# Kernel optimization log

Hardware: AMD Instinct MI355X
Metric: run time of the kernel (lower is better)

The kernel has to match this reference:

```python
import jax, jax.numpy as jnp
import numpy as np

V, E, SH, H = 10004, 300, 1024, 512
B, T = 128, 50
PAD = 10003


def setup_inputs() -> dict:
    key = jax.random.key(0)
    ks = jax.random.split(key, 13)
    s = 0.05
    emb = s * jax.random.normal(ks[0], (V, E), dtype=jnp.float32)
    emb = emb.at[PAD].set(0.0)  # padding_idx row is zero
    G = 2 * H  # GRU hidden size is 2*hid_size
    Wih = s * jax.random.normal(ks[1], (3 * G, E), dtype=jnp.float32)
    Whh = s * jax.random.normal(ks[2], (3 * G, G), dtype=jnp.float32)
    bih = s * jax.random.normal(ks[3], (3 * G,), dtype=jnp.float32)
    bhh = s * jax.random.normal(ks[4], (3 * G,), dtype=jnp.float32)
    W1 = s * jax.random.normal(ks[5], (H, SH), dtype=jnp.float32)
    b1 = s * jax.random.normal(ks[6], (H,), dtype=jnp.float32)
    W2 = s * jax.random.normal(ks[7], (E, G), dtype=jnp.float32)
    b2 = s * jax.random.normal(ks[8], (E,), dtype=jnp.float32)
    Wout = s * jax.random.normal(ks[9], (V, E), dtype=jnp.float32)
    ses_encoding = jax.random.normal(ks[10], (1, B, SH), dtype=jnp.float32)
    x = jax.random.randint(ks[11], (B, T), 0, 10000)
    return {"ses_encoding": ses_encoding, "x": x, "emb": emb, "Wih": Wih,
            "Whh": Whh, "bih": bih, "bhh": bhh, "W1": W1, "b1": b1,
            "W2": W2, "b2": b2, "Wout": Wout}


def reference(ses_encoding, x, emb, Wih, Whh, bih, bhh, W1, b1, W2, b2, Wout):
    hid = W1.shape[0]            # hid_size
    G = Whh.shape[1]             # 2*hid_size (GRU hidden)
    # ses_encoding = tanh(lin1(ses_encoding)), then viewed to [1, B, hid]
    ses = jnp.tanh(jnp.einsum('lbs,hs->lbh', ses_encoding, W1) + b1)[0]  # [B, hid]
    emb_all = emb[x]             # [B, T, E] (dropout inactive at eval)

    def step(h, e_t):
        # GRU hidden input each step: concat(prev_half, ses) -> [B, 2*hid]
        Hfull = jnp.concatenate([h, ses], axis=-1)
        gx = e_t @ Wih.T + bih                      # [B, 3G]
        gh = Hfull @ Whh.T + bhh                    # [B, 3G]
        r = jax.nn.sigmoid(gx[:, :G] + gh[:, :G])
        z = jax.nn.sigmoid(gx[:, G:2 * G] + gh[:, G:2 * G])
        n = jnp.tanh(gx[:, 2 * G:] + r * gh[:, 2 * G:])
        hnew = (1.0 - z) * n + z * Hfull            # [B, 2*hid]
        o = hnew @ W2.T + b2 + e_t                  # lin2(hid_o) + residual emb
        logits = o @ Wout.T                         # [B, V]
        return hnew[:, :hid], logits

    _, logits = jax.lax.scan(step, ses, jnp.swapaxes(emb_all, 0, 1))
    return jnp.swapaxes(logits, 0, 1)               # [B, T, V]
```

## Files before the change

### kernel.cpp

```cpp
#include <hip/hip_runtime.h>


typedef __bf16 bf16x8 __attribute__((ext_vector_type(8)));
typedef float f32x4 __attribute__((ext_vector_type(4)));
typedef unsigned long long u64;

struct CvtAll {
    const float* src[7];
    int srows[7], scols[7], sstride[7], soff[7], drows[7], dcols[7];
    __bf16* dst[7];
    int blk0[8];
    const int* x; const float* emb; __bf16* embbf;
};

__global__ void cvt_all_kernel(CvtAll p) {
    int bid = blockIdx.x;
    if (bid >= p.blk0[7]) {
        int idx = (bid - p.blk0[7]) * 256 + threadIdx.x;
        if (idx >= 6400 * 320) return;
        int m = idx / 320, c = idx - m * 320;
        int t = m >> 7, b = m & 127;
        int tok = p.x[b * 50 + t];
        float v = (c < 300) ? p.emb[(size_t)tok * 300 + c] : 0.0f;
        p.embbf[idx] = (__bf16)v;
        return;
    }
    int s = 0;
    while (s < 6 && bid >= p.blk0[s + 1]) ++s;
    int idx = (bid - p.blk0[s]) * 256 + threadIdx.x;
    int dc = p.dcols[s];
    int r = idx / dc, c = idx - r * dc;
    if (r >= p.drows[s]) return;
    float v = 0.0f;
    if (r < p.srows[s] && c < p.scols[s])
        v = p.src[s][(size_t)r * p.sstride[s] + p.soff[s] + c];
    p.dst[s][(size_t)r * dc + c] = (__bf16)v;
}

struct GemmParams {
    const __bf16* A; int lda;
    const __bf16* B; int ldb; int Brows;
    int K;
    const float* bias;
    float* outF; int ldo; int Nstore;
    __bf16* outBf;
    const __bf16* res;
    const float* add2;
    int ld2; int add2lim;
};

template <int EPI>
__launch_bounds__(256, 2)
__global__ void gemm_bt(GemmParams p) {
    __shared__ __bf16 As[128][72];
    __shared__ __bf16 Bs[128][72];

    const int tid = threadIdx.x;
    const int lane = tid & 63;
    const int wid = tid >> 6;
    const int wr = wid >> 1, wc = wid & 1;
    const int m0 = blockIdx.x * 128, c0 = blockIdx.y * 128;
    const int lrow = lane & 15;
    const int kq = lane >> 4;

    int srow[4], scol[4];
#pragma unroll
    for (int i = 0; i < 4; ++i) {
        int chunk = i * 256 + tid;
        srow[i] = chunk >> 3;
        scol[i] = (chunk & 7) * 8;
    }

    f32x4 acc[4][4];
#pragma unroll
    for (int i = 0; i < 4; ++i)
#pragma unroll
        for (int j = 0; j < 4; ++j) acc[i][j] = (f32x4){0.f, 0.f, 0.f, 0.f};

    const int nkb = p.K >> 6;
    bf16x8 ra[4], rb[4];
#pragma unroll
    for (int i = 0; i < 4; ++i) {
        ra[i] = *reinterpret_cast<const bf16x8*>(
            p.A + (size_t)(m0 + srow[i]) * p.lda + scol[i]);
        bf16x8 z;
#pragma unroll
        for (int q = 0; q < 8; ++q) z[q] = (__bf16)0.0f;
        int grow = c0 + srow[i];
        rb[i] = (grow < p.Brows)
            ? *reinterpret_cast<const bf16x8*>(p.B + (size_t)grow * p.ldb + scol[i])
            : z;
    }

    for (int kb = 0; kb < nkb; ++kb) {
        __syncthreads();
#pragma unroll
        for (int i = 0; i < 4; ++i) {
            *reinterpret_cast<bf16x8*>(&As[srow[i]][scol[i]]) = ra[i];
            *reinterpret_cast<bf16x8*>(&Bs[srow[i]][scol[i]]) = rb[i];
        }
        __syncthreads();

        if (kb + 1 < nkb) {
            int ko = (kb + 1) << 6;
#pragma unroll
            for (int i = 0; i < 4; ++i) {
                ra[i] = *reinterpret_cast<const bf16x8*>(
                    p.A + (size_t)(m0 + srow[i]) * p.lda + ko + scol[i]);
                bf16x8 z;
#pragma unroll
                for (int q = 0; q < 8; ++q) z[q] = (__bf16)0.0f;
                int grow = c0 + srow[i];
                rb[i] = (grow < p.Brows)
                    ? *reinterpret_cast<const bf16x8*>(
                          p.B + (size_t)grow * p.ldb + ko + scol[i])
                    : z;
            }
        }

#pragma unroll
        for (int kk = 0; kk < 2; ++kk) {
            bf16x8 af[4], bfr[4];
#pragma unroll
            for (int m = 0; m < 4; ++m)
                af[m] = *reinterpret_cast<const bf16x8*>(
                    &As[wr * 64 + m * 16 + lrow][kk * 32 + kq * 8]);
#pragma unroll
            for (int n = 0; n < 4; ++n)
                bfr[n] = *reinterpret_cast<const bf16x8*>(
                    &Bs[wc * 64 + n * 16 + lrow][kk * 32 + kq * 8]);
#pragma unroll
            for (int m = 0; m < 4; ++m)
#pragma unroll
                for (int n = 0; n < 4; ++n)
                    acc[m][n] = __builtin_amdgcn_mfma_f32_16x16x32_bf16(
                        af[m], bfr[n], acc[m][n], 0, 0, 0);
        }
    }

#pragma unroll
    for (int m = 0; m < 4; ++m) {
#pragma unroll
        for (int n = 0; n < 4; ++n) {
#pragma unroll
            for (int i = 0; i < 4; ++i) {
                int r = m0 + wr * 64 + m * 16 + kq * 4 + i;
                int c = c0 + wc * 64 + n * 16 + lrow;
                float v = acc[m][n][i];
                if constexpr (EPI == 1) {
                    v = tanhf(v + p.bias[c]);
                    p.outBf[(size_t)r * p.ldo + c] = (__bf16)v;
                    p.outF[(size_t)c * 128 + r] = v;
                } else if constexpr (EPI == 2) {
                    int ro = (r & 127) * 50 + (r >> 7);
                    if (c < 300) {
                        v += p.bias[c] + (float)p.res[(size_t)r * 320 + c];
                        p.outBf[(size_t)ro * 320 + c] = (__bf16)v;
                    } else if (c < 320) {
                        p.outBf[(size_t)ro * 320 + c] = (__bf16)0.0f;
                    }
                } else if constexpr (EPI == 3) {
                    if (c < p.Nstore) p.outF[(size_t)r * p.ldo + c] = v;
                } else {
                    if (c < p.Brows) {
                        float v2 = v + p.bias[r];
                        if (p.add2 && r < p.add2lim)
                            v2 += p.add2[(size_t)r * 128 + (c & 127)];
                        p.outF[(size_t)(c >> 7) * p.ldo + (size_t)r * 128 + (c & 127)] = v2;
                    }
                }
            }
        }
    }
}

#define SCAN_NB 64
__launch_bounds__(256, 1)
__global__ void scan_kernel(const __bf16* __restrict__ Whh_a,
                            const float* __restrict__ gxT,
                            const float* __restrict__ ghcT,
                            const float* __restrict__ sesT,
                            u64* __restrict__ F,
                            unsigned* __restrict__ cnt) {
    __shared__ char smem[131072];
    char* Ws = smem;
    char* Hs = smem + 98304;
    const int tid = threadIdx.x;
    const int lane = tid & 63;
    const int wid = tid >> 6;
    const int wr = wid >> 1, wc = wid & 1;
    const int bid = blockIdx.x;
    const int q = bid >> 4;
    const int j0 = (bid & 15) * 32;
    const int lrow = lane & 15, kq = lane >> 4;

    for (int it = 0; it < 24; ++it) {
        int c = it * 256 + tid;
        int rl = c >> 6, o16 = c & 63;
        int g = rl >> 5, jj = rl & 31;
        bf16x8 v = *reinterpret_cast<const bf16x8*>(
            Whh_a + (size_t)(g * 1024 + j0 + jj) * 512 + o16 * 8);
        *reinterpret_cast<bf16x8*>(Ws + rl * 1024 + ((o16 * 16) ^ ((rl & 7) << 4))) = v;
    }

    const int b_g = q * 32 + wc * 16 + lrow;
    const int jbase = j0 + wr * 16 + kq * 4;

    float cn[4], hprev[4], gcur[12], gpre[12];
#pragma unroll
    for (int i = 0; i < 4; ++i) {
        cn[i] = ghcT[(size_t)(2048 + jbase + i) * 128 + b_g];
        hprev[i] = sesT[(size_t)(jbase + i) * 128 + b_g];
    }
#pragma unroll
    for (int i = 0; i < 4; ++i) {
        gpre[i]     = gxT[(size_t)(jbase + i) * 128 + b_g];
        gpre[4 + i] = gxT[(size_t)(1024 + jbase + i) * 128 + b_g];
        gpre[8 + i] = gxT[(size_t)(2048 + jbase + i) * 128 + b_g];
    }

    for (int t = 0; t < 50; ++t) {
        for (int it = 0; it < 16; ++it) {
            int c = it * 256 + tid;
            int rl = c >> 7, o8 = c & 127;
            u64 v = __hip_atomic_load(
                F + ((size_t)t * 128 + q * 32 + rl) * 256 + o8,
                __ATOMIC_RELAXED, __HIP_MEMORY_SCOPE_AGENT);
            *reinterpret_cast<u64*>(Hs + rl * 1024 + ((o8 * 8) ^ ((rl & 7) << 4))) = v;
        }
#pragma unroll
        for (int i = 0; i < 12; ++i) gcur[i] = gpre[i];
        {
            int tn = (t < 49) ? t + 1 : 49;
            const float* gxt = gxT + (size_t)tn * 3072 * 128;
#pragma unroll
            for (int i = 0; i < 4; ++i) {
                gpre[i]     = gxt[(size_t)(jbase + i) * 128 + b_g];
                gpre[4 + i] = gxt[(size_t)(1024 + jbase + i) * 128 + b_g];
                gpre[8 + i] = gxt[(size_t)(2048 + jbase + i) * 128 + b_g];
            }
        }
        asm volatile("s_waitcnt lgkmcnt(0)\n\ts_barrier" ::: "memory");
        __builtin_amdgcn_sched_barrier(0);

        f32x4 acc[3];
#pragma unroll
        for (int g = 0; g < 3; ++g) acc[g] = (f32x4){0.f, 0.f, 0.f, 0.f};
        const int hrow = wc * 16 + lrow;
        const int arow0 = wr * 16 + lrow;
        for (int kb = 0; kb < 16; ++kb) {
            int ko = kb * 64 + kq * 16;
            bf16x8 hfrag = *reinterpret_cast<const bf16x8*>(
                Hs + hrow * 1024 + (ko ^ ((hrow & 7) << 4)));
#pragma unroll
            for (int g = 0; g < 3; ++g) {
                int arow = g * 32 + arow0;
                bf16x8 wfrag = *reinterpret_cast<const bf16x8*>(
                    Ws + arow * 1024 + (ko ^ ((arow & 7) << 4)));
                acc[g] = __builtin_amdgcn_mfma_f32_16x16x32_bf16(
                    wfrag, hfrag, acc[g], 0, 0, 0);
            }
        }

        union { u64 u; __bf16 h[4]; } pk;
#pragma unroll
        for (int i = 0; i < 4; ++i) {
            float r = 1.0f / (1.0f + expf(-(gcur[i] + acc[0][i])));
            float z = 1.0f / (1.0f + expf(-(gcur[4 + i] + acc[1][i])));
            float nn = tanhf(gcur[8 + i] + r * (acc[2][i] + cn[i]));
            float hn = (1.0f - z) * nn + z * hprev[i];
            hprev[i] = hn;
            pk.h[i] = (__bf16)hn;
        }
        __hip_atomic_store(
            F + ((size_t)(t + 1) * 128 + b_g) * 256 + (jbase >> 2), pk.u,
            __ATOMIC_RELAXED, __HIP_MEMORY_SCOPE_AGENT);

        if (t < 49) {
            __syncthreads();
            if (tid == 0) {
                __hip_atomic_fetch_add(cnt + q * 32, 1u,
                                       __ATOMIC_RELAXED, __HIP_MEMORY_SCOPE_AGENT);
                unsigned tgt = (unsigned)(t + 1) * 16u;
                while (__hip_atomic_load(cnt + q * 32, __ATOMIC_RELAXED,
                                         __HIP_MEMORY_SCOPE_AGENT) < tgt)
                    __builtin_amdgcn_s_sleep(1);
            }
            __syncthreads();
        }
    }
}

__launch_bounds__(256, 1)
__global__ void tail_kernel(const __bf16* __restrict__ Whh_a,
                            const float* __restrict__ gxT,
                            const float* __restrict__ ghcT,
                            const float* __restrict__ sesT,
                            __bf16* __restrict__ F) {
    __shared__ char smem[131072];
    char* Ws = smem;
    char* Hs = smem + 98304;
    const int tid = threadIdx.x;
    const int lane = tid & 63;
    const int wid = tid >> 6;
    const int wr = wid >> 1, wc = wid & 1;
    const int bid = blockIdx.x;
    const int tseg = bid >> 6;
    const int rem = bid & 63;
    const int q = rem >> 4;
    const int j0 = 512 + (rem & 15) * 32;
    const int lrow = lane & 15, kq = lane >> 4;

    const int t0 = (tseg < 2) ? tseg * 13 : 26 + (tseg - 2) * 12;
    const int t1 = (tseg < 2) ? t0 + 13 : t0 + 12;

    for (int it = 0; it < 24; ++it) {
        int c = it * 256 + tid;
        int rl = c >> 6, o16 = c & 63;
        int g = rl >> 5, jj = rl & 31;
        bf16x8 v = *reinterpret_cast<const bf16x8*>(
            Whh_a + (size_t)(g * 1024 + j0 + jj) * 512 + o16 * 8);
        *reinterpret_cast<bf16x8*>(Ws + rl * 1024 + ((o16 * 16) ^ ((rl & 7) << 4))) = v;
    }

    const int b_g = q * 32 + wc * 16 + lrow;
    const int jbase = j0 + wr * 16 + kq * 4;

    float cn[4], sv[4];
#pragma unroll
    for (int i = 0; i < 4; ++i) {
        cn[i] = ghcT[(size_t)(2048 + jbase + i) * 128 + b_g];
        sv[i] = sesT[(size_t)(jbase + i - 512) * 128 + b_g];
    }

    for (int tt = t0; tt < t1; ++tt) {
        for (int it = 0; it < 8; ++it) {
            int c = it * 256 + tid;
            int rl = c >> 6, o16 = c & 63;
            bf16x8 v = *reinterpret_cast<const bf16x8*>(
                F + ((size_t)tt * 128 + q * 32 + rl) * 1024 + o16 * 8);
            *reinterpret_cast<bf16x8*>(Hs + rl * 1024 + ((o16 * 16) ^ ((rl & 7) << 4))) = v;
        }
        const float* gxt = gxT + (size_t)tt * 3072 * 128;
        float g0[12];
#pragma unroll
        for (int i = 0; i < 4; ++i) {
            g0[i]     = gxt[(size_t)(jbase + i) * 128 + b_g];
            g0[4 + i] = gxt[(size_t)(1024 + jbase + i) * 128 + b_g];
            g0[8 + i] = gxt[(size_t)(2048 + jbase + i) * 128 + b_g];
        }
        __syncthreads();

        f32x4 acc[3];
#pragma unroll
        for (int g = 0; g < 3; ++g) acc[g] = (f32x4){0.f, 0.f, 0.f, 0.f};
        const int hrow = wc * 16 + lrow;
        const int arow0 = wr * 16 + lrow;
        for (int kb = 0; kb < 16; ++kb) {
            int ko = kb * 64 + kq * 16;
            bf16x8 hfrag = *reinterpret_cast<const bf16x8*>(
                Hs + hrow * 1024 + (ko ^ ((hrow & 7) << 4)));
#pragma unroll
            for (int g = 0; g < 3; ++g) {
                int arow = g * 32 + arow0;
                bf16x8 wfrag = *reinterpret_cast<const bf16x8*>(
                    Ws + arow * 1024 + (ko ^ ((arow & 7) << 4)));
                acc[g] = __builtin_amdgcn_mfma_f32_16x16x32_bf16(
                    wfrag, hfrag, acc[g], 0, 0, 0);
            }
        }

        union { u64 u; __bf16 h[4]; } pk;
#pragma unroll
        for (int i = 0; i < 4; ++i) {
            float r = 1.0f / (1.0f + expf(-(g0[i] + acc[0][i])));
            float z = 1.0f / (1.0f + expf(-(g0[4 + i] + acc[1][i])));
            float nn = tanhf(g0[8 + i] + r * (acc[2][i] + cn[i]));
            pk.h[i] = (__bf16)((1.0f - z) * nn + z * sv[i]);
        }
        *reinterpret_cast<u64*>(F + ((size_t)(tt + 1) * 128 + b_g) * 1024 + jbase) = pk.u;
        __syncthreads();
    }
}

extern "C" void kernel_launch(void* const* d_in, const int* in_sizes, int n_in,
                              void* d_out, int out_size, void* d_ws, size_t ws_size,
                              hipStream_t stream) {
    const float* ses_enc = (const float*)d_in[0];
    const int*   x       = (const int*)d_in[1];
    const float* emb     = (const float*)d_in[2];
    const float* Wih     = (const float*)d_in[3];
    const float* Whh     = (const float*)d_in[4];
    const float* bih     = (const float*)d_in[5];
    const float* bhh     = (const float*)d_in[6];
    const float* W1      = (const float*)d_in[7];
    const float* b1      = (const float*)d_in[8];
    const float* W2      = (const float*)d_in[9];
    const float* b2      = (const float*)d_in[10];
    const float* Wout    = (const float*)d_in[11];
    float* out = (float*)d_out;

    char* ws = (char*)d_ws;
    float*  sesT      = (float*)(ws + 0);
    float*  ghcT      = (float*)(ws + 262144);
    __bf16* o_bf      = (__bf16*)(ws + 1835008);
    __bf16* W1_bf     = (__bf16*)(ws + 5931008);
    __bf16* Whh_a_bf  = (__bf16*)(ws + 6979584);
    __bf16* Whh_b_bf  = (__bf16*)(ws + 10125312);
    __bf16* Wih_bf    = (__bf16*)(ws + 13271040);
    __bf16* W2_bf     = (__bf16*)(ws + 15237120);
    __bf16* Wout_bf   = (__bf16*)(ws + 15851520);
    __bf16* sesenc_bf = (__bf16*)(ws + 22323200);
    unsigned* cnt     = (unsigned*)(ws + 22585344);

    char* ob = (char*)d_out;
    float*  gxT     = (float*)ob;
    __bf16* emb_bf  = (__bf16*)(ob + 80000000);
    __bf16* F       = (__bf16*)(ob + 88000000);

    dim3 blk(256);

    CvtAll ca;
    const float* csrc[7]  = {W1, Whh, Whh, Wih, W2, Wout, ses_enc};
    int csr[7]  = {512, 3072, 3072, 3072, 300, 10004, 128};
    int csc[7]  = {1024, 512, 512, 300, 1024, 300, 1024};
    int cst[7]  = {1024, 1024, 1024, 300, 1024, 300, 1024};
    int cso[7]  = {0, 0, 512, 0, 0, 0, 0};
    __bf16* cdst[7] = {W1_bf, Whh_a_bf, Whh_b_bf, Wih_bf, W2_bf, Wout_bf, sesenc_bf};
    int cdr[7]  = {512, 3072, 3072, 3072, 300, 10112, 128};
    int cdc[7]  = {1024, 512, 512, 320, 1024, 320, 1024};
    int b0 = 0;
    for (int s = 0; s < 7; ++s) {
        ca.src[s] = csrc[s]; ca.srows[s] = csr[s]; ca.scols[s] = csc[s];
        ca.sstride[s] = cst[s]; ca.soff[s] = cso[s];
        ca.dst[s] = cdst[s]; ca.drows[s] = cdr[s]; ca.dcols[s] = cdc[s];
        ca.blk0[s] = b0;
        b0 += (cdr[s] * cdc[s] + 255) / 256;
    }
    ca.blk0[7] = b0;
    ca.x = x; ca.emb = emb; ca.embbf = emb_bf;
    int total_blocks = b0 + (6400 * 320) / 256;
    cvt_all_kernel<<<total_blocks, 256, 0, stream>>>(ca);
    hipMemsetAsync(cnt, 0, 1024, stream);

    GemmParams P;

    P = {sesenc_bf, 1024, W1_bf, 1024, 512, 1024, b1, sesT, 1024, 512, F,
         nullptr, nullptr, 0, 0};
    gemm_bt<1><<<dim3(1, 4), blk, 0, stream>>>(P);

    P = {Whh_b_bf, 512, F, 1024, 128, 512, bhh, ghcT, 0, 0, nullptr,
         nullptr, nullptr, 0, 0};
    gemm_bt<4><<<dim3(24, 1), blk, 0, stream>>>(P);

    P = {Wih_bf, 320, emb_bf, 320, 6400, 320, bih, gxT, 3072 * 128, 0, nullptr,
         nullptr, ghcT, 0, 2048};
    gemm_bt<4><<<dim3(24, 50), blk, 0, stream>>>(P);

    scan_kernel<<<SCAN_NB, 256, 0, stream>>>(
        Whh_a_bf, gxT, ghcT, sesT, (u64*)F, cnt);

    tail_kernel<<<256, 256, 0, stream>>>(Whh_a_bf, gxT, ghcT, sesT, F);

    P = {F + 128 * 1024, 1024, W2_bf, 1024, 300, 1024, b2, nullptr, 0, 300, o_bf,
         emb_bf, nullptr, 0, 0};
    gemm_bt<2><<<dim3(50, 3), blk, 0, stream>>>(P);

    P = {o_bf, 320, Wout_bf, 320, 10112, 320, nullptr, out, 10004, 10004, nullptr,
         nullptr, nullptr, 0, 0};
    gemm_bt<3><<<dim3(50, 79), blk, 0, stream>>>(P);

    (void)in_sizes; (void)n_in; (void)out_size; (void)ws_size;
}
```

Baseline: 630.5 us.

## Fold tail GRU half into scan kernel, overlapping it with inter-block barrier wait

Removes the separate tail kernel that computed the second (non-recurrent) half of the GRU output columns. The scan kernel now computes those columns each step in the window between signalling its arrival counter and spinning on the grid barrier, so that work hides the synchronisation latency. The extra weights are read straight from global memory instead of LDS, which adds global traffic inside the serial loop and register pressure. The write into F for the second half uses a packed u64 layout, so downstream consumers must agree with that indexing.

```diff
diff --git a/kernel.cpp b/kernel.cpp
--- a/kernel.cpp
+++ b/kernel.cpp
@@ -204,19 +204,26 @@
     }
 
     const int b_g = q * 32 + wc * 16 + lrow;
-    const int jbase = j0 + wr * 16 + kq * 4;
+    const int jbase  = j0 + wr * 16 + kq * 4;
+    const int jbase2 = 512 + j0 + wr * 16 + kq * 4;
 
     float cn[4], hprev[4], gcur[12], gpre[12];
+    float cn2[4], sv2[4], gcur2[12], gpre2[12];
 #pragma unroll
     for (int i = 0; i < 4; ++i) {
-        cn[i] = ghcT[(size_t)(2048 + jbase + i) * 128 + b_g];
+        cn[i]  = ghcT[(size_t)(2048 + jbase + i) * 128 + b_g];
         hprev[i] = sesT[(size_t)(jbase + i) * 128 + b_g];
+        cn2[i] = ghcT[(size_t)(2048 + jbase2 + i) * 128 + b_g];
+        sv2[i] = sesT[(size_t)(jbase2 - 512 + i) * 128 + b_g];
     }
 #pragma unroll
     for (int i = 0; i < 4; ++i) {
-        gpre[i]     = gxT[(size_t)(jbase + i) * 128 + b_g];
-        gpre[4 + i] = gxT[(size_t)(1024 + jbase + i) * 128 + b_g];
-        gpre[8 + i] = gxT[(size_t)(2048 + jbase + i) * 128 + b_g];
+        gpre[i]      = gxT[(size_t)(jbase + i) * 128 + b_g];
+        gpre[4 + i]  = gxT[(size_t)(1024 + jbase + i) * 128 + b_g];
+        gpre[8 + i]  = gxT[(size_t)(2048 + jbase + i) * 128 + b_g];
+        gpre2[i]     = gxT[(size_t)(jbase2 + i) * 128 + b_g];
+        gpre2[4 + i] = gxT[(size_t)(1024 + jbase2 + i) * 128 + b_g];
+        gpre2[8 + i] = gxT[(size_t)(2048 + jbase2 + i) * 128 + b_g];
     }
 
     for (int t = 0; t < 50; ++t) {
@@ -229,15 +236,18 @@
             *reinterpret_cast<u64*>(Hs + rl * 1024 + ((o8 * 8) ^ ((rl & 7) << 4))) = v;
         }
 #pragma unroll
-        for (int i = 0; i < 12; ++i) gcur[i] = gpre[i];
+        for (int i = 0; i < 12; ++i) { gcur[i] = gpre[i]; gcur2[i] = gpre2[i]; }
         {
             int tn = (t < 49) ? t + 1 : 49;
             const float* gxt = gxT + (size_t)tn * 3072 * 128;
 #pragma unroll
             for (int i = 0; i < 4; ++i) {
-                gpre[i]     = gxt[(size_t)(jbase + i) * 128 + b_g];
-                gpre[4 + i] = gxt[(size_t)(1024 + jbase + i) * 128 + b_g];
-                gpre[8 + i] = gxt[(size_t)(2048 + jbase + i) * 128 + b_g];
+                gpre[i]      = gxt[(size_t)(jbase + i) * 128 + b_g];
+                gpre[4 + i]  = gxt[(size_t)(1024 + jbase + i) * 128 + b_g];
+                gpre[8 + i]  = gxt[(size_t)(2048 + jbase + i) * 128 + b_g];
+                gpre2[i]     = gxt[(size_t)(jbase2 + i) * 128 + b_g];
+                gpre2[4 + i] = gxt[(size_t)(1024 + jbase2 + i) * 128 + b_g];
+                gpre2[8 + i] = gxt[(size_t)(2048 + jbase2 + i) * 128 + b_g];
             }
         }
         asm volatile("s_waitcnt lgkmcnt(0)\n\ts_barrier" ::: "memory");
@@ -278,9 +288,41 @@
 
         if (t < 49) {
             __syncthreads();
-            if (tid == 0) {
+            if (tid == 0)
                 __hip_atomic_fetch_add(cnt + q * 32, 1u,
                                        __ATOMIC_RELAXED, __HIP_MEMORY_SCOPE_AGENT);
+        }
+
+        {
+            f32x4 acc2[3];
+#pragma unroll
+            for (int g = 0; g < 3; ++g) acc2[g] = (f32x4){0.f, 0.f, 0.f, 0.f};
+            for (int kb = 0; kb < 16; ++kb) {
+                int ko = kb * 64 + kq * 16;
+                bf16x8 hfrag = *reinterpret_cast<const bf16x8*>(
+                    Hs + hrow * 1024 + (ko ^ ((hrow & 7) << 4)));
+#pragma unroll
+                for (int g = 0; g < 3; ++g) {
+                    bf16x8 af2 = *reinterpret_cast<const bf16x8*>(
+                        Whh_a + (size_t)(g * 1024 + 512 + j0 + wr * 16 + lrow) * 512
+                              + kb * 32 + kq * 8);
+                    acc2[g] = __builtin_amdgcn_mfma_f32_16x16x32_bf16(
+                        af2, hfrag, acc2[g], 0, 0, 0);
+                }
+            }
+            union { u64 u; __bf16 h[4]; } pk2;
+#pragma unroll
+            for (int i = 0; i < 4; ++i) {
+                float r = 1.0f / (1.0f + expf(-(gcur2[i] + acc2[0][i])));
+                float z = 1.0f / (1.0f + expf(-(gcur2[4 + i] + acc2[1][i])));
+                float nn = tanhf(gcur2[8 + i] + r * (acc2[2][i] + cn2[i]));
+                pk2.h[i] = (__bf16)((1.0f - z) * nn + z * sv2[i]);
+            }
+            F[((size_t)(t + 1) * 128 + b_g) * 256 + 128 + ((jbase2 - 512) >> 2)] = pk2.u;
+        }
+
+        if (t < 49) {
+            if (tid == 0) {
                 unsigned tgt = (unsigned)(t + 1) * 16u;
                 while (__hip_atomic_load(cnt + q * 32, __ATOMIC_RELAXED,
                                          __HIP_MEMORY_SCOPE_AGENT) < tgt)
@@ -288,98 +330,6 @@
             }
             __syncthreads();
         }
-    }
-}
-
-__launch_bounds__(256, 1)
-__global__ void tail_kernel(const __bf16* __restrict__ Whh_a,
-                            const float* __restrict__ gxT,
-                            const float* __restrict__ ghcT,
-                            const float* __restrict__ sesT,
-                            __bf16* __restrict__ F) {
-    __shared__ char smem[131072];
-    char* Ws = smem;
-    char* Hs = smem + 98304;
-    const int tid = threadIdx.x;
-    const int lane = tid & 63;
-    const int wid = tid >> 6;
-    const int wr = wid >> 1, wc = wid & 1;
-    const int bid = blockIdx.x;
-    const int tseg = bid >> 6;
-    const int rem = bid & 63;
-    const int q = rem >> 4;
-    const int j0 = 512 + (rem & 15) * 32;
-    const int lrow = lane & 15, kq = lane >> 4;
-
-    const int t0 = (tseg < 2) ? tseg * 13 : 26 + (tseg - 2) * 12;
-    const int t1 = (tseg < 2) ? t0 + 13 : t0 + 12;
-
-    for (int it = 0; it < 24; ++it) {
-        int c = it * 256 + tid;
-        int rl = c >> 6, o16 = c & 63;
-        int g = rl >> 5, jj = rl & 31;
-        bf16x8 v = *reinterpret_cast<const bf16x8*>(
-            Whh_a + (size_t)(g * 1024 + j0 + jj) * 512 + o16 * 8);
-        *reinterpret_cast<bf16x8*>(Ws + rl * 1024 + ((o16 * 16) ^ ((rl & 7) << 4))) = v;
-    }
-
-    const int b_g = q * 32 + wc * 16 + lrow;
-    const int jbase = j0 + wr * 16 + kq * 4;
-
-    float cn[4], sv[4];
-#pragma unroll
-    for (int i = 0; i < 4; ++i) {
-        cn[i] = ghcT[(size_t)(2048 + jbase + i) * 128 + b_g];
-        sv[i] = sesT[(size_t)(jbase + i - 512) * 128 + b_g];
-    }
-
-    for (int tt = t0; tt < t1; ++tt) {
-        for (int it = 0; it < 8; ++it) {
-            int c = it * 256 + tid;
-            int rl = c >> 6, o16 = c & 63;
-            bf16x8 v = *reinterpret_cast<const bf16x8*>(
-                F + ((size_t)tt * 128 + q * 32 + rl) * 1024 + o16 * 8);
-            *reinterpret_cast<bf16x8*>(Hs + rl * 1024 + ((o16 * 16) ^ ((rl & 7) << 4))) = v;
-        }
-        const float* gxt = gxT + (size_t)tt * 3072 * 128;
-        float g0[12];
-#pragma unroll
-        for (int i = 0; i < 4; ++i) {
-            g0[i]     = gxt[(size_t)(jbase + i) * 128 + b_g];
-            g0[4 + i] = gxt[(size_t)(1024 + jbase + i) * 128 + b_g];
-            g0[8 + i] = gxt[(size_t)(2048 + jbase + i) * 128 + b_g];
-        }
-        __syncthreads();
-
-        f32x4 acc[3];
-#pragma unroll
-        for (int g = 0; g < 3; ++g) acc[g] = (f32x4){0.f, 0.f, 0.f, 0.f};
-        const int hrow = wc * 16 + lrow;
-        const int arow0 = wr * 16 + lrow;
-        for (int kb = 0; kb < 16; ++kb) {
-            int ko = kb * 64 + kq * 16;
-            bf16x8 hfrag = *reinterpret_cast<const bf16x8*>(
-                Hs + hrow * 1024 + (ko ^ ((hrow & 7) << 4)));
-#pragma unroll
-            for (int g = 0; g < 3; ++g) {
-                int arow = g * 32 + arow0;
-                bf16x8 wfrag = *reinterpret_cast<const bf16x8*>(
-                    Ws + arow * 1024 + (ko ^ ((arow & 7) << 4)));
-                acc[g] = __builtin_amdgcn_mfma_f32_16x16x32_bf16(
-                    wfrag, hfrag, acc[g], 0, 0, 0);
-            }
-        }
-
-        union { u64 u; __bf16 h[4]; } pk;
-#pragma unroll
-        for (int i = 0; i < 4; ++i) {
-            float r = 1.0f / (1.0f + expf(-(g0[i] + acc[0][i])));
-            float z = 1.0f / (1.0f + expf(-(g0[4 + i] + acc[1][i])));
-            float nn = tanhf(g0[8 + i] + r * (acc[2][i] + cn[i]));
-            pk.h[i] = (__bf16)((1.0f - z) * nn + z * sv[i]);
-        }
-        *reinterpret_cast<u64*>(F + ((size_t)(tt + 1) * 128 + b_g) * 1024 + jbase) = pk.u;
-        __syncthreads();
     }
 }
 
@@ -460,8 +410,6 @@
     scan_kernel<<<SCAN_NB, 256, 0, stream>>>(
         Whh_a_bf, gxT, ghcT, sesT, (u64*)F, cnt);
 
-    tail_kernel<<<256, 256, 0, stream>>>(Whh_a_bf, gxT, ghcT, sesT, F);
-
     P = {F + 128 * 1024, 1024, W2_bf, 1024, 300, 1024, b2, nullptr, 0, 300, o_bf,
          emb_bf, nullptr, 0, 0};
     gemm_bt<2><<<dim3(50, 3), blk, 0, stream>>>(P);
```

New measurement: 913.0 us. 44.8% more time.
